# Optimization experiments

Hardware: AMD Instinct MI355X
Metric: run time of the kernel (lower is better)

The kernel has to match this reference:

```python
import jax, jax.numpy as jnp
import numpy as np

GAMMA = 1.1


def setup_inputs() -> dict:
    key = jax.random.key(0)
    k1, k2 = jax.random.split(key)
    points = jax.random.normal(k1, (262144, 5), dtype=jnp.float32)  # x,y,z,intensity,time
    boxes = jax.random.normal(k2, (256, 9), dtype=jnp.float32)      # x,y,z,dx,dy,dz,heading,vx,vy
    return {"points": points, "boxes": boxes, "num_sample": 128}


def reference(points, boxes, num_sample):
    """Cylindrical pooling ('even' branch of VoxelSampler.cylindrical_pool).

    points: [N, C] float, boxes: [M, 9] float. Returns [M, num_sample, C+2].
    """
    # per-box cylindrical radius from box footprint half-extent
    radii = jnp.linalg.norm(boxes[:, 3:5] * 0.5, axis=-1) * GAMMA          # [M]
    # pairwise BEV distance between box centers and points
    diff = boxes[:, None, :2] - points[None, :, :2]                         # [M, N, 2]
    dis = jnp.linalg.norm(diff, axis=-1)                                    # [M, N]
    point_mask = (dis <= radii[:, None]).astype(points.dtype)               # [M, N] 0/1
    # topk over the binary mask: picks up to num_sample in-radius points per box
    sampled_mask, sampled_idx = jax.lax.top_k(point_mask, num_sample)       # [M, S]
    sampled_points = points[sampled_idx]                                    # [M, S, C]
    # append box velocity (last 2 box dims) to each sampled point
    vel = jnp.broadcast_to(boxes[:, None, -2:],
                           (boxes.shape[0], num_sample, 2))                 # [M, S, 2]
    out = jnp.concatenate([sampled_points, vel], axis=-1)                   # [M, S, C+2]
    # zero out slots that were not actually inside the radius
    out = jnp.where(sampled_mask[..., None] > 0, out, jnp.zeros((), out.dtype))
    return out
```

## Files before the change

kernel.cpp:

```cpp
#include <hip/hip_runtime.h>
#include <hip/hip_bf16.h>
#include <math.h>


#define P0GRP 128

__device__ __forceinline__ float box_radius(const float* __restrict__ b) {
    float hx = __fmul_rn(b[3], 0.5f);
    float hy = __fmul_rn(b[4], 0.5f);
    float nrm = __fsqrt_rn(__fadd_rn(__fmul_rn(hx, hx), __fmul_rn(hy, hy)));
    return __fmul_rn(nrm, 1.1f);
}

__device__ float sqrt_le_threshold(float r) {
    float x = __fmul_rn(r, r);
    #pragma unroll 1
    for (int i = 0; i < 16; ++i) {
        float nx = nextafterf(x, INFINITY);
        if (__fsqrt_rn(nx) <= r) x = nx; else break;
    }
    #pragma unroll 1
    for (int i = 0; i < 16; ++i) {
        if (__fsqrt_rn(x) <= r) break;
        x = nextafterf(x, -INFINITY);
    }
    return x;
}

__device__ __forceinline__ bool pt_in(float bx, float by, float T,
                                      float px, float py) {
    float dx = __fsub_rn(bx, px);
    float dy = __fsub_rn(by, py);
    float d2 = __fadd_rn(__fmul_rn(dx, dx), __fmul_rn(dy, dy));
    return d2 <= T;
}

__global__ __launch_bounds__(1024) void kernelA(
    const float* __restrict__ pts, const float* __restrict__ boxes,
    int* __restrict__ counts, float4* __restrict__ bprep,
    float* __restrict__ out, int N, int M, int S, int ngrp, int ngrpA) {
    extern __shared__ int s_work[];
    __shared__ int s_cnt[P0GRP];
    __shared__ int s_tot[16];
    __shared__ int s_wtot[2];
    __shared__ int s_nwork;

    int m = blockIdx.x;
    int tid = threadIdx.x;
    int lane = tid & 63;
    int wid = tid >> 6;

    const float* b = boxes + (size_t)m * 9;
    float bx = b[0], by = b[1];
    float T = sqrt_le_threshold(box_radius(b));
    float vx = b[7], vy = b[8];

    if (tid == 0) s_nwork = 0;

    int tot = 0;
    for (int g = wid; g < ngrpA; g += 16) {
        int p = g * 64 + lane;
        bool v = p < N;
        float px = v ? pts[(size_t)p * 5 + 0] : 3.0e38f;
        float py = v ? pts[(size_t)p * 5 + 1] : 3.0e38f;
        int c = __popcll(__ballot(pt_in(bx, by, T, px, py)));
        if (lane == 0) s_cnt[g] = c;
        tot += c;
    }
    if (lane == 0) s_tot[wid] = tot;
    __syncthreads();

    int total = 0;
    #pragma unroll
    for (int w = 0; w < 16; ++w) total += s_tot[w];

    if (tid == 0) bprep[m] = make_float4(bx, by, T, __int_as_float(total));
    bool unsat = total < S;
    if (unsat) {
        for (int g = tid; g < ngrpA; g += 1024)
            counts[(size_t)m * ngrp + g] = s_cnt[g];
        if (ngrpA != ngrp) return;
    }

    int c = (tid < ngrpA) ? s_cnt[tid] : 0;
    int incl = c;
    if (wid < 2) {
        #pragma unroll
        for (int d = 1; d < 64; d <<= 1) {
            int u = __shfl_up(incl, d, 64);
            if (lane >= d) incl += u;
        }
        if (lane == 63) s_wtot[wid] = incl;
    }
    __syncthreads();
    if (tid < ngrpA) {
        int base = incl - c + (wid == 1 ? s_wtot[0] : 0);
        if (c > 0 && base < S) {
            int slot = atomicAdd(&s_nwork, 1);
            s_work[slot] = (base << 16) | tid;
        }
    }
    __syncthreads();
    int nwork = s_nwork;

    for (int i = wid; i < nwork; i += 16) {
        int e = s_work[i];
        int g = e & 0xffff;
        int gbase = e >> 16;
        int p = g * 64 + lane;
        bool in = false;
        float px = 0.f, py = 0.f;
        if (p < N) {
            px = pts[(size_t)p * 5 + 0];
            py = pts[(size_t)p * 5 + 1];
            in = pt_in(bx, by, T, px, py);
        }
        unsigned long long bal = __ballot(in);
        int rank = __popcll(bal & ((1ull << lane) - 1ull));
        int pos = gbase + rank;
        if (in && pos < S) {
            float* o = out + ((size_t)m * S + pos) * 7;
            const float* pp = pts + (size_t)p * 5;
            o[0] = px;    o[1] = py;    o[2] = pp[2];
            o[3] = pp[3]; o[4] = pp[4];
            o[5] = vx;    o[6] = vy;
        }
    }

    int cnt = total < S ? total : S;
    size_t outbase = (size_t)m * S * 7;
    for (int i = cnt * 7 + tid; i < S * 7; i += 1024) out[outbase + i] = 0.0f;
}

__global__ __launch_bounds__(256) void kernelB(
    const float* __restrict__ pts, const float4* __restrict__ bprep,
    int* __restrict__ counts, int N, int M, int S, int ngrp, int ngrpA,
    int ntile, int mchunk) {
    __shared__ float4 s_box[64];
    __shared__ unsigned long long s_mask;
    int tid = threadIdx.x;
    int lane = tid & 63;
    int wid = tid >> 6;

    int tile = blockIdx.x % ntile;
    int mc = blockIdx.x / ntile;
    int m0 = mc * mchunk;
    int nmb = M - m0; if (nmb > mchunk) nmb = mchunk;

    bool act = false;
    if (tid < nmb) {
        float4 bb = bprep[m0 + tid];
        s_box[tid] = bb;
        act = __float_as_int(bb.w) < S;
    }
    unsigned long long bal = __ballot(act);
    if (tid == 0) s_mask = bal;
    __syncthreads();
    unsigned long long amask = s_mask;
    if (amask == 0) return;

    int pbase = ngrpA * 64 + tile * 1024 + wid * 256;
    int g0 = pbase >> 6;
    if (g0 >= ngrp) return;
    bool vec4 = (g0 + 4 <= ngrp);

    float px[4], py[4];
    #pragma unroll
    for (int i = 0; i < 4; ++i) {
        int p = pbase + i * 64 + lane;
        bool v = p < N;
        px[i] = v ? pts[(size_t)p * 5 + 0] : 3.0e38f;
        py[i] = v ? pts[(size_t)p * 5 + 1] : 3.0e38f;
    }

    while (amask) {
        int mm = __builtin_ctzll(amask);
        amask &= amask - 1;
        float4 bb = s_box[mm];
        int cnt[4];
        #pragma unroll
        for (int i = 0; i < 4; ++i)
            cnt[i] = __popcll(__ballot(pt_in(bb.x, bb.y, bb.z, px[i], py[i])));
        if (lane == 0) {
            int* dst = counts + (size_t)(m0 + mm) * ngrp + g0;
            if (vec4) {
                *reinterpret_cast<int4*>(dst) =
                    make_int4(cnt[0], cnt[1], cnt[2], cnt[3]);
            } else {
                #pragma unroll
                for (int i = 0; i < 4; ++i)
                    if (g0 + i < ngrp) dst[i] = cnt[i];
            }
        }
    }
}

__global__ __launch_bounds__(1024) void kernelC(
    const float* __restrict__ pts, const float* __restrict__ boxes,
    const float4* __restrict__ bprep,
    const int* __restrict__ counts, float* __restrict__ out,
    int N, int M, int S, int ngrp) {
    extern __shared__ int s_work[];
    __shared__ int s_wsum[16];
    __shared__ int s_nwork;

    int m = blockIdx.x;
    float4 bb = bprep[m];
    int satA = __float_as_int(bb.w);
    if (satA >= S) return;

    int tid = threadIdx.x;
    int lane = tid & 63;
    int wid = tid >> 6;

    if (tid == 0) s_nwork = 0;

    float bx = bb.x, by = bb.y, T = bb.z;
    float vx = boxes[(size_t)m * 9 + 7];
    float vy = boxes[(size_t)m * 9 + 8];

    const int* my_counts = counts + (size_t)m * ngrp;
    int gpt = (ngrp + 1023) >> 10;
    int g0 = tid * gpt;

    int c[8];
    int tsum = 0;
    if (gpt == 4 && (g0 & 3) == 0 && g0 + 3 < ngrp) {
        int4 v4 = *reinterpret_cast<const int4*>(my_counts + g0);
        c[0] = v4.x; c[1] = v4.y; c[2] = v4.z; c[3] = v4.w;
        tsum = c[0] + c[1] + c[2] + c[3];
    } else {
        #pragma unroll
        for (int i = 0; i < 8; ++i) {
            int g = g0 + i;
            c[i] = (i < gpt && g < ngrp) ? my_counts[g] : 0;
            tsum += c[i];
        }
    }

    int v = tsum;
    #pragma unroll
    for (int d = 1; d < 64; d <<= 1) {
        int u = __shfl_up(v, d, 64);
        if (lane >= d) v += u;
    }
    if (lane == 63) s_wsum[wid] = v;
    __syncthreads();

    int woff = 0, total = 0;
    #pragma unroll
    for (int w = 0; w < 16; ++w) {
        int s = s_wsum[w];
        total += s;
        if (w < wid) woff += s;
    }
    int base = woff + (v - tsum);

    for (int i = 0; i < gpt; ++i) {
        int g = g0 + i;
        if (g < ngrp) {
            int cnt = c[i];
            if (cnt > 0 && base < S) {
                int slot = atomicAdd(&s_nwork, 1);
                s_work[slot] = (base << 16) | g;
            }
            base += cnt;
        }
    }
    __syncthreads();
    int nwork = s_nwork;

    for (int i = wid; i < nwork; i += 16) {
        int e = s_work[i];
        int g = e & 0xffff;
        int gbase = e >> 16;
        int p = g * 64 + lane;
        bool in = false;
        float px = 0.f, py = 0.f;
        if (p < N) {
            px = pts[(size_t)p * 5 + 0];
            py = pts[(size_t)p * 5 + 1];
            in = pt_in(bx, by, T, px, py);
        }
        unsigned long long bal = __ballot(in);
        int rank = __popcll(bal & ((1ull << lane) - 1ull));
        int pos = gbase + rank;
        if (in && pos < S) {
            float* o = out + ((size_t)m * S + pos) * 7;
            const float* pp = pts + (size_t)p * 5;
            o[0] = px;    o[1] = py;    o[2] = pp[2];
            o[3] = pp[3]; o[4] = pp[4];
            o[5] = vx;    o[6] = vy;
        }
    }

    int cnt = total < S ? total : S;
    size_t outbase = (size_t)m * S * 7;
    for (int i = cnt * 7 + tid; i < S * 7; i += 1024) out[outbase + i] = 0.0f;
}

__global__ __launch_bounds__(256) void simple_kernel(
    const float* __restrict__ pts, const float* __restrict__ boxes,
    float* __restrict__ out, int N, int M, int S) {
    __shared__ int s_wc[4];
    int m = blockIdx.x;
    int tid = threadIdx.x;
    int lane = tid & 63;
    int wid = tid >> 6;

    const float* b = boxes + (size_t)m * 9;
    float bx = b[0], by = b[1];
    float T = sqrt_le_threshold(box_radius(b));
    float vx = b[7], vy = b[8];

    int base = 0;
    for (int start = 0; start < N && base < S; start += 256) {
        int p = start + tid;
        bool in = false;
        if (p < N) {
            float px = pts[(size_t)p * 5 + 0];
            float py = pts[(size_t)p * 5 + 1];
            in = pt_in(bx, by, T, px, py);
        }
        unsigned long long bal = __ballot(in);
        if (lane == 0) s_wc[wid] = __popcll(bal);
        __syncthreads();
        int off = 0;
        for (int w = 0; w < wid; ++w) off += s_wc[w];
        int pos = base + off + __popcll(bal & ((1ull << lane) - 1ull));
        if (in && pos < S) {
            float* o = out + ((size_t)m * S + pos) * 7;
            const float* pp = pts + (size_t)p * 5;
            o[0] = pp[0]; o[1] = pp[1]; o[2] = pp[2];
            o[3] = pp[3]; o[4] = pp[4];
            o[5] = vx;    o[6] = vy;
        }
        base += s_wc[0] + s_wc[1] + s_wc[2] + s_wc[3];
        __syncthreads();
    }

    int cnt = base < S ? base : S;
    size_t outbase = (size_t)m * S * 7;
    for (int i = cnt * 7 + tid; i < S * 7; i += 256) out[outbase + i] = 0.0f;
}

extern "C" void kernel_launch(void* const* d_in, const int* in_sizes, int n_in,
                              void* d_out, int out_size, void* d_ws, size_t ws_size,
                              hipStream_t stream) {
    const float* pts = (const float*)d_in[0];
    const float* boxes = (const float*)d_in[1];
    float* out = (float*)d_out;

    int N = in_sizes[0] / 5;
    int M = in_sizes[1] / 9;
    int S = out_size / (M * 7);
    int ngrp = (N + 63) / 64;
    int ngrpA = ngrp < P0GRP ? ngrp : P0GRP;

    size_t counts_bytes = ((size_t)M * ngrp * sizeof(int) + 15) & ~(size_t)15;
    size_t need = counts_bytes + (size_t)M * sizeof(float4);

    if (ws_size >= need && S < 32768 && ngrp <= 4096) {
        int* counts = (int*)d_ws;
        float4* bprep = (float4*)((char*)d_ws + counts_bytes);
        size_t lds = (size_t)(S + 64) * sizeof(int);

        kernelA<<<M, 1024, lds, stream>>>(pts, boxes, counts, bprep, out,
                                          N, M, S, ngrp, ngrpA);

        if (ngrp > ngrpA) {
            int ntile = (ngrp - ngrpA + 15) / 16;
            int msplit = 2048 / ntile;
            if (msplit < 1) msplit = 1;
            if (msplit > M) msplit = M;
            int mchunk = (M + msplit - 1) / msplit;
            if (mchunk > 64) mchunk = 64;
            msplit = (M + mchunk - 1) / mchunk;
            kernelB<<<ntile * msplit, 256, 0, stream>>>(
                pts, bprep, counts, N, M, S, ngrp, ngrpA, ntile, mchunk);

            kernelC<<<M, 1024, lds, stream>>>(pts, boxes, bprep, counts, out,
                                              N, M, S, ngrp);
        }
    } else {
        simple_kernel<<<M, 256, 0, stream>>>(pts, boxes, out, N, M, S);
    }
}
```

Baseline: 26.97 us.

## Move saturated-box gather into counting kernel and compute threshold with warp ballot

New measurement: 29.41 us. +9.0%, slower.

```diff
diff --git a/kernel.cpp b/kernel.cpp
--- a/kernel.cpp
+++ b/kernel.cpp
@@ -12,19 +12,14 @@
     return __fmul_rn(nrm, 1.1f);
 }
 
-__device__ float sqrt_le_threshold(float r) {
-    float x = __fmul_rn(r, r);
-    #pragma unroll 1
-    for (int i = 0; i < 16; ++i) {
-        float nx = nextafterf(x, INFINITY);
-        if (__fsqrt_rn(nx) <= r) x = nx; else break;
-    }
-    #pragma unroll 1
-    for (int i = 0; i < 16; ++i) {
-        if (__fsqrt_rn(x) <= r) break;
-        x = nextafterf(x, -INFINITY);
-    }
-    return x;
+__device__ __forceinline__ float probe_T(float r, int lane) {
+    int xb = __float_as_int(__fmul_rn(r, r));
+    int yb = xb + lane - 32; if (yb < 0) yb = 0;
+    bool ok = __fsqrt_rn(__int_as_float(yb)) <= r;
+    unsigned long long mask = __ballot(ok);
+    int hi = 63 - __clzll(mask);
+    int tb = xb + hi - 32; if (tb < 0) tb = 0;
+    return __int_as_float(tb);
 }
 
 __device__ __forceinline__ bool pt_in(float bx, float by, float T,
@@ -38,13 +33,8 @@
 __global__ __launch_bounds__(1024) void kernelA(
     const float* __restrict__ pts, const float* __restrict__ boxes,
     int* __restrict__ counts, float4* __restrict__ bprep,
-    float* __restrict__ out, int N, int M, int S, int ngrp, int ngrpA) {
-    extern __shared__ int s_work[];
-    __shared__ int s_cnt[P0GRP];
+    int N, int M, int ngrp, int ngrpA) {
     __shared__ int s_tot[16];
-    __shared__ int s_wtot[2];
-    __shared__ int s_nwork;
-
     int m = blockIdx.x;
     int tid = threadIdx.x;
     int lane = tid & 63;
@@ -52,10 +42,7 @@
 
     const float* b = boxes + (size_t)m * 9;
     float bx = b[0], by = b[1];
-    float T = sqrt_le_threshold(box_radius(b));
-    float vx = b[7], vy = b[8];
-
-    if (tid == 0) s_nwork = 0;
+    float T = probe_T(box_radius(b), lane);
 
     int tot = 0;
     for (int g = wid; g < ngrpA; g += 16) {
@@ -64,40 +51,219 @@
         float px = v ? pts[(size_t)p * 5 + 0] : 3.0e38f;
         float py = v ? pts[(size_t)p * 5 + 1] : 3.0e38f;
         int c = __popcll(__ballot(pt_in(bx, by, T, px, py)));
-        if (lane == 0) s_cnt[g] = c;
+        if (lane == 0) counts[(size_t)m * ngrp + g] = c;
         tot += c;
     }
     if (lane == 0) s_tot[wid] = tot;
     __syncthreads();
-
-    int total = 0;
+    if (tid == 0) {
+        int total = 0;
+        #pragma unroll
+        for (int w = 0; w < 16; ++w) total += s_tot[w];
+        bprep[m] = make_float4(bx, by, T, __int_as_float(total));
+    }
+}
+
+__global__ __launch_bounds__(256) void kernelB(
+    const float* __restrict__ pts, const float* __restrict__ boxes,
+    const float4* __restrict__ bprep, int* __restrict__ counts,
+    float* __restrict__ out,
+    int N, int M, int S, int ngrp, int ngrpA, int ntile, int mchunk, int TB) {
+    extern __shared__ int s_work[];
+    __shared__ float4 s_box[64];
+    __shared__ unsigned long long s_mask;
+    __shared__ int s_ws[4];
+    __shared__ int s_nwork;
+
+    int bid = blockIdx.x;
+    int tid = threadIdx.x;
+    int lane = tid & 63;
+    int wid = tid >> 6;
+
+    if (bid < TB) {
+        int tile = bid % ntile;
+        int mc = bid / ntile;
+        int m0 = mc * mchunk;
+        int nmb = M - m0; if (nmb > mchunk) nmb = mchunk;
+
+        bool act = false;
+        if (tid < nmb) {
+            float4 bb = bprep[m0 + tid];
+            s_box[tid] = bb;
+            act = __float_as_int(bb.w) < S;
+        }
+        unsigned long long bal = __ballot(act);
+        if (tid == 0) s_mask = bal;
+        __syncthreads();
+        unsigned long long amask = s_mask;
+        if (amask == 0) return;
+
+        int pbase = ngrpA * 64 + tile * 1024 + wid * 256;
+        int g0 = pbase >> 6;
+        if (g0 >= ngrp) return;
+        bool vec4 = (g0 + 4 <= ngrp);
+
+        float px[4], py[4];
+        #pragma unroll
+        for (int i = 0; i < 4; ++i) {
+            int p = pbase + i * 64 + lane;
+            bool v = p < N;
+            px[i] = v ? pts[(size_t)p * 5 + 0] : 3.0e38f;
+            py[i] = v ? pts[(size_t)p * 5 + 1] : 3.0e38f;
+        }
+        while (amask) {
+            int mm = __builtin_ctzll(amask);
+            amask &= amask - 1;
+            float4 bb = s_box[mm];
+            int cnt[4];
+            #pragma unroll
+            for (int i = 0; i < 4; ++i)
+                cnt[i] = __popcll(__ballot(pt_in(bb.x, bb.y, bb.z,
+                                                 px[i], py[i])));
+            if (lane == 0) {
+                int* dst = counts + (size_t)(m0 + mm) * ngrp + g0;
+                if (vec4) {
+                    *reinterpret_cast<int4*>(dst) =
+                        make_int4(cnt[0], cnt[1], cnt[2], cnt[3]);
+                } else {
+                    #pragma unroll
+                    for (int i = 0; i < 4; ++i)
+                        if (g0 + i < ngrp) dst[i] = cnt[i];
+                }
+            }
+        }
+        return;
+    }
+
+    int m = bid - TB;
+    float4 bb = bprep[m];
+    int satA = __float_as_int(bb.w);
+    if (satA < S) return;
+
+    if (tid == 0) s_nwork = 0;
+    float bx = bb.x, by = bb.y, T = bb.z;
+    float vx = boxes[(size_t)m * 9 + 7];
+    float vy = boxes[(size_t)m * 9 + 8];
+    const int* my_counts = counts + (size_t)m * ngrp;
+
+    int c = (tid < ngrpA) ? my_counts[tid] : 0;
+    int v = c;
     #pragma unroll
-    for (int w = 0; w < 16; ++w) total += s_tot[w];
-
-    if (tid == 0) bprep[m] = make_float4(bx, by, T, __int_as_float(total));
-    bool unsat = total < S;
-    if (unsat) {
-        for (int g = tid; g < ngrpA; g += 1024)
-            counts[(size_t)m * ngrp + g] = s_cnt[g];
-        if (ngrpA != ngrp) return;
-    }
-
-    int c = (tid < ngrpA) ? s_cnt[tid] : 0;
-    int incl = c;
-    if (wid < 2) {
+    for (int d = 1; d < 64; d <<= 1) {
+        int u = __shfl_up(v, d, 64);
+        if (lane >= d) v += u;
+    }
+    if (lane == 63) s_ws[wid] = v;
+    __syncthreads();
+    int woff = 0;
+    #pragma unroll
+    for (int w = 0; w < 4; ++w) if (w < wid) woff += s_ws[w];
+    int base = woff + (v - c);
+
+    if (tid < ngrpA && c > 0 && base < S) {
+        int slot = atomicAdd(&s_nwork, 1);
+        s_work[slot] = (base << 16) | tid;
+    }
+    __syncthreads();
+    int nwork = s_nwork;
+
+    for (int i = wid; i < nwork; i += 4) {
+        int e = s_work[i];
+        int g = e & 0xffff;
+        int gbase = e >> 16;
+        int p = g * 64 + lane;
+        bool in = false;
+        float px = 0.f, py = 0.f;
+        if (p < N) {
+            px = pts[(size_t)p * 5 + 0];
+            py = pts[(size_t)p * 5 + 1];
+            in = pt_in(bx, by, T, px, py);
+        }
+        unsigned long long bal = __ballot(in);
+        int rank = __popcll(bal & ((1ull << lane) - 1ull));
+        int pos = gbase + rank;
+        if (in && pos < S) {
+            float* o = out + ((size_t)m * S + pos) * 7;
+            const float* pp = pts + (size_t)p * 5;
+            o[0] = px;    o[1] = py;    o[2] = pp[2];
+            o[3] = pp[3]; o[4] = pp[4];
+            o[5] = vx;    o[6] = vy;
+        }
+    }
+}
+
+__global__ __launch_bounds__(1024) void kernelC(
+    const float* __restrict__ pts, const float* __restrict__ boxes,
+    const float4* __restrict__ bprep,
+    const int* __restrict__ counts, float* __restrict__ out,
+    int N, int M, int S, int ngrp) {
+    extern __shared__ int s_work[];
+    __shared__ int s_wsum[16];
+    __shared__ int s_nwork;
+
+    int m = blockIdx.x;
+    float4 bb = bprep[m];
+    int satA = __float_as_int(bb.w);
+    if (satA >= S) return;
+
+    int tid = threadIdx.x;
+    int lane = tid & 63;
+    int wid = tid >> 6;
+
+    if (tid == 0) s_nwork = 0;
+    float bx = bb.x, by = bb.y, T = bb.z;
+    float vx = boxes[(size_t)m * 9 + 7];
+    float vy = boxes[(size_t)m * 9 + 8];
+
+    const int* my_counts = counts + (size_t)m * ngrp;
+    int gpt = (ngrp + 1023) >> 10;
+    int g0 = tid * gpt;
+
+    int c[4];
+    int tsum = 0;
+    if (gpt == 4 && ((ngrp & 3) == 0) && g0 + 3 < ngrp) {
+        int4 v4 = *reinterpret_cast<const int4*>(my_counts + g0);
+        c[0] = v4.x; c[1] = v4.y; c[2] = v4.z; c[3] = v4.w;
+        tsum = c[0] + c[1] + c[2] + c[3];
+    } else {
         #pragma unroll
-        for (int d = 1; d < 64; d <<= 1) {
-            int u = __shfl_up(incl, d, 64);
-            if (lane >= d) incl += u;
-        }
-        if (lane == 63) s_wtot[wid] = incl;
-    }
+        for (int i = 0; i < 4; ++i) {
+            int g = g0 + i;
+            c[i] = (i < gpt && g < ngrp) ? my_counts[g] : 0;
+            tsum += c[i];
+        }
+    }
+
+    int v = tsum;
+    #pragma unroll
+    for (int d = 1; d < 64; d <<= 1) {
+        int u = __shfl_up(v, d, 64);
+        if (lane >= d) v += u;
+    }
+    if (lane == 63) s_wsum[wid] = v;
     __syncthreads();
-    if (tid < ngrpA) {
-        int base = incl - c + (wid == 1 ? s_wtot[0] : 0);
-        if (c > 0 && base < S) {
-            int slot = atomicAdd(&s_nwork, 1);
-            s_work[slot] = (base << 16) | tid;
+
+    int woff = 0, total = 0;
+    #pragma unroll
+    for (int w = 0; w < 16; ++w) {
+        int s = s_wsum[w];
+        total += s;
+        if (w < wid) woff += s;
+    }
+    int base = woff + (v - tsum);
+
+    #pragma unroll
+    for (int i = 0; i < 4; ++i) {
+        if (i < gpt) {
+            int g = g0 + i;
+            if (g < ngrp) {
+                int cnt = c[i];
+                if (cnt > 0 && base < S) {
+                    int slot = atomicAdd(&s_nwork, 1);
+                    s_work[slot] = (base << 16) | g;
+                }
+                base += cnt;
+            }
         }
     }
     __syncthreads();
@@ -132,171 +298,19 @@
     for (int i = cnt * 7 + tid; i < S * 7; i += 1024) out[outbase + i] = 0.0f;
 }
 
-__global__ __launch_bounds__(256) void kernelB(
-    const float* __restrict__ pts, const float4* __restrict__ bprep,
-    int* __restrict__ counts, int N, int M, int S, int ngrp, int ngrpA,
-    int ntile, int mchunk) {
-    __shared__ float4 s_box[64];
-    __shared__ unsigned long long s_mask;
-    int tid = threadIdx.x;
-    int lane = tid & 63;
-    int wid = tid >> 6;
-
-    int tile = blockIdx.x % ntile;
-    int mc = blockIdx.x / ntile;
-    int m0 = mc * mchunk;
-    int nmb = M - m0; if (nmb > mchunk) nmb = mchunk;
-
-    bool act = false;
-    if (tid < nmb) {
-        float4 bb = bprep[m0 + tid];
-        s_box[tid] = bb;
-        act = __float_as_int(bb.w) < S;
-    }
-    unsigned long long bal = __ballot(act);
-    if (tid == 0) s_mask = bal;
-    __syncthreads();
-    unsigned long long amask = s_mask;
-    if (amask == 0) return;
-
-    int pbase = ngrpA * 64 + tile * 1024 + wid * 256;
-    int g0 = pbase >> 6;
-    if (g0 >= ngrp) return;
-    bool vec4 = (g0 + 4 <= ngrp);
-
-    float px[4], py[4];
-    #pragma unroll
-    for (int i = 0; i < 4; ++i) {
-        int p = pbase + i * 64 + lane;
-        bool v = p < N;
-        px[i] = v ? pts[(size_t)p * 5 + 0] : 3.0e38f;
-        py[i] = v ? pts[(size_t)p * 5 + 1] : 3.0e38f;
-    }
-
-    while (amask) {
-        int mm = __builtin_ctzll(amask);
-        amask &= amask - 1;
-        float4 bb = s_box[mm];
-        int cnt[4];
-        #pragma unroll
-        for (int i = 0; i < 4; ++i)
-            cnt[i] = __popcll(__ballot(pt_in(bb.x, bb.y, bb.z, px[i], py[i])));
-        if (lane == 0) {
-            int* dst = counts + (size_t)(m0 + mm) * ngrp + g0;
-            if (vec4) {
-                *reinterpret_cast<int4*>(dst) =
-                    make_int4(cnt[0], cnt[1], cnt[2], cnt[3]);
-            } else {
-                #pragma unroll
-                for (int i = 0; i < 4; ++i)
-                    if (g0 + i < ngrp) dst[i] = cnt[i];
-            }
-        }
-    }
-}
-
-__global__ __launch_bounds__(1024) void kernelC(
-    const float* __restrict__ pts, const float* __restrict__ boxes,
-    const float4* __restrict__ bprep,
-    const int* __restrict__ counts, float* __restrict__ out,
-    int N, int M, int S, int ngrp) {
-    extern __shared__ int s_work[];
-    __shared__ int s_wsum[16];
-    __shared__ int s_nwork;
-
-    int m = blockIdx.x;
-    float4 bb = bprep[m];
-    int satA = __float_as_int(bb.w);
-    if (satA >= S) return;
-
-    int tid = threadIdx.x;
-    int lane = tid & 63;
-    int wid = tid >> 6;
-
-    if (tid == 0) s_nwork = 0;
-
-    float bx = bb.x, by = bb.y, T = bb.z;
-    float vx = boxes[(size_t)m * 9 + 7];
-    float vy = boxes[(size_t)m * 9 + 8];
-
-    const int* my_counts = counts + (size_t)m * ngrp;
-    int gpt = (ngrp + 1023) >> 10;
-    int g0 = tid * gpt;
-
-    int c[8];
-    int tsum = 0;
-    if (gpt == 4 && (g0 & 3) == 0 && g0 + 3 < ngrp) {
-        int4 v4 = *reinterpret_cast<const int4*>(my_counts + g0);
-        c[0] = v4.x; c[1] = v4.y; c[2] = v4.z; c[3] = v4.w;
-        tsum = c[0] + c[1] + c[2] + c[3];
-    } else {
-        #pragma unroll
-        for (int i = 0; i < 8; ++i) {
-            int g = g0 + i;
-            c[i] = (i < gpt && g < ngrp) ? my_counts[g] : 0;
-            tsum += c[i];
-        }
-    }
-
-    int v = tsum;
-    #pragma unroll
-    for (int d = 1; d < 64; d <<= 1) {
-        int u = __shfl_up(v, d, 64);
-        if (lane >= d) v += u;
-    }
-    if (lane == 63) s_wsum[wid] = v;
-    __syncthreads();
-
-    int woff = 0, total = 0;
-    #pragma unroll
-    for (int w = 0; w < 16; ++w) {
-        int s = s_wsum[w];
-        total += s;
-        if (w < wid) woff += s;
-    }
-    int base = woff + (v - tsum);
-
-    for (int i = 0; i < gpt; ++i) {
-        int g = g0 + i;
-        if (g < ngrp) {
-            int cnt = c[i];
-            if (cnt > 0 && base < S) {
-                int slot = atomicAdd(&s_nwork, 1);
-                s_work[slot] = (base << 16) | g;
-            }
-            base += cnt;
-        }
-    }
-    __syncthreads();
-    int nwork = s_nwork;
-
-    for (int i = wid; i < nwork; i += 16) {
-        int e = s_work[i];
-        int g = e & 0xffff;
-        int gbase = e >> 16;
-        int p = g * 64 + lane;
-        bool in = false;
-        float px = 0.f, py = 0.f;
-        if (p < N) {
-            px = pts[(size_t)p * 5 + 0];
-            py = pts[(size_t)p * 5 + 1];
-            in = pt_in(bx, by, T, px, py);
-        }
-        unsigned long long bal = __ballot(in);
-        int rank = __popcll(bal & ((1ull << lane) - 1ull));
-        int pos = gbase + rank;
-        if (in && pos < S) {
-            float* o = out + ((size_t)m * S + pos) * 7;
-            const float* pp = pts + (size_t)p * 5;
-            o[0] = px;    o[1] = py;    o[2] = pp[2];
-            o[3] = pp[3]; o[4] = pp[4];
-            o[5] = vx;    o[6] = vy;
-        }
-    }
-
-    int cnt = total < S ? total : S;
-    size_t outbase = (size_t)m * S * 7;
-    for (int i = cnt * 7 + tid; i < S * 7; i += 1024) out[outbase + i] = 0.0f;
+__device__ float sqrt_le_threshold(float r) {
+    float x = __fmul_rn(r, r);
+    #pragma unroll 1
+    for (int i = 0; i < 16; ++i) {
+        float nx = nextafterf(x, INFINITY);
+        if (__fsqrt_rn(nx) <= r) x = nx; else break;
+    }
+    #pragma unroll 1
+    for (int i = 0; i < 16; ++i) {
+        if (__fsqrt_rn(x) <= r) break;
+        x = nextafterf(x, -INFINITY);
+    }
+    return x;
 }
 
 __global__ __launch_bounds__(256) void simple_kernel(
@@ -360,28 +374,31 @@
     size_t counts_bytes = ((size_t)M * ngrp * sizeof(int) + 15) & ~(size_t)15;
     size_t need = counts_bytes + (size_t)M * sizeof(float4);
 
-    if (ws_size >= need && S < 32768 && ngrp <= 4096) {
+    if (ws_size >= need && S >= 1 && S < 32768 && ngrp <= 4096 && M <= 65535) {
         int* counts = (int*)d_ws;
         float4* bprep = (float4*)((char*)d_ws + counts_bytes);
         size_t lds = (size_t)(S + 64) * sizeof(int);
 
-        kernelA<<<M, 1024, lds, stream>>>(pts, boxes, counts, bprep, out,
-                                          N, M, S, ngrp, ngrpA);
-
+        kernelA<<<M, 1024, 0, stream>>>(pts, boxes, counts, bprep,
+                                        N, M, ngrp, ngrpA);
+
+        int ntile = 0, mchunk = 1, TB = 0;
         if (ngrp > ngrpA) {
-            int ntile = (ngrp - ngrpA + 15) / 16;
+            ntile = (ngrp - ngrpA + 15) / 16;
             int msplit = 2048 / ntile;
             if (msplit < 1) msplit = 1;
             if (msplit > M) msplit = M;
-            int mchunk = (M + msplit - 1) / msplit;
+            mchunk = (M + msplit - 1) / msplit;
             if (mchunk > 64) mchunk = 64;
             msplit = (M + mchunk - 1) / mchunk;
-            kernelB<<<ntile * msplit, 256, 0, stream>>>(
-                pts, bprep, counts, N, M, S, ngrp, ngrpA, ntile, mchunk);
-
-            kernelC<<<M, 1024, lds, stream>>>(pts, boxes, bprep, counts, out,
-                                              N, M, S, ngrp);
-        }
+            TB = ntile * msplit;
+        }
+        kernelB<<<TB + M, 256, lds, stream>>>(pts, boxes, bprep, counts, out,
+                                              N, M, S, ngrp, ngrpA,
+                                              ntile, mchunk, TB);
+
+        kernelC<<<M, 1024, lds, stream>>>(pts, boxes, bprep, counts, out,
+                                          N, M, S, ngrp);
     } else {
         simple_kernel<<<M, 256, 0, stream>>>(pts, boxes, out, N, M, S);
     }
```
